# Kernel tuning notes

Measured on AMD Instinct MI355X. Metric: run time of the kernel, lower is better.

Reference implementation:

```python
import jax, jax.numpy as jnp
import numpy as np

B, S, HID, H = 4, 2048, 1024, 8
D = HID // H  # per-head dim = 128


def setup_inputs() -> dict:
    key = jax.random.key(0)
    ks = jax.random.split(key, 8)
    q = jax.random.normal(ks[0], (B, S, HID), dtype=jnp.float32)
    k = jax.random.normal(ks[1], (B, S, HID), dtype=jnp.float32)
    v = jax.random.normal(ks[2], (B, S, HID), dtype=jnp.float32)
    mask = jax.random.randint(ks[3], (B, S), 0, 2, dtype=jnp.int32)  # 1 = masked key
    # Linear(hidden, hidden, bias=False) weights, stored [in, out] so y = x @ W
    xavier = lambda kk: jax.random.uniform(kk, (HID, HID), jnp.float32,
                                           -np.sqrt(6.0 / (2 * HID)), np.sqrt(6.0 / (2 * HID)))
    return {"q": q, "k": k, "v": v, "mask": mask,
            "Wq": xavier(ks[4]), "Wk": xavier(ks[5]), "Wv": xavier(ks[6]), "Wo": xavier(ks[7])}


def reference(q, k, v, mask, Wq, Wk, Wv, Wo):
    scale = D ** -0.5
    # project and split heads: [B,S,HID] -> [B,H,S,D]
    qq = (q @ Wq).reshape(B, S, H, D).transpose(0, 2, 1, 3) * scale
    kk = (k @ Wk).reshape(B, S, H, D).transpose(0, 2, 1, 3)
    vv = (v @ Wv).reshape(B, S, H, D).transpose(0, 2, 1, 3)
    # scores [B,H,Sq,Sk]; mask broadcasts over heads and query rows (key padding)
    scores = jnp.einsum('bhqd,bhkd->bhqk', qq, kk)
    scores = jnp.where(mask.astype(bool)[:, None, None, :], jnp.float32(-1e9), scores)
    attn = jax.nn.softmax(scores, axis=-1)  # dropout_rate=0 (eval) -> identity
    ctx = jnp.einsum('bhqk,bhkd->bhqd', attn, vv)
    out = ctx.transpose(0, 2, 1, 3).reshape(B, S, HID) @ Wo
    return out, attn
```

## Files before the change

kernel.cpp:

```cpp
#include <hip/hip_runtime.h>
#include <hip/hip_bf16.h>

#define HIDN 1024
#define NH   8
#define DH   128
#define BB   4
#define SS   2048

typedef __bf16 bf16;
typedef bf16 bf16x4 __attribute__((ext_vector_type(4)));
typedef bf16 bf16x8 __attribute__((ext_vector_type(8)));
typedef float f32x4 __attribute__((ext_vector_type(4)));

#if __has_builtin(__builtin_amdgcn_exp2f)
#define EXP2(x) __builtin_amdgcn_exp2f(x)
#else
#define EXP2(x) exp2f(x)
#endif

static __device__ inline f32x4 mfma16(bf16x8 a, bf16x8 b, f32x4 c) {
    return __builtin_amdgcn_mfma_f32_16x16x32_bf16(a, b, c, 0, 0, 0);
}

static __device__ inline void gload_lds16(const void* g, void* l) {
    __builtin_amdgcn_global_load_lds(
        (const __attribute__((address_space(1))) unsigned int*)g,
        (__attribute__((address_space(3))) unsigned int*)l, 16, 0, 0);
}

__global__ void cvt_kernel(const float* __restrict__ q, const float* __restrict__ k,
                           const float* __restrict__ v,
                           bf16* __restrict__ qo, bf16* __restrict__ ko, bf16* __restrict__ vo) {
    const float* src = blockIdx.y == 0 ? q : blockIdx.y == 1 ? k : v;
    bf16* dst = blockIdx.y == 0 ? qo : blockIdx.y == 1 ? ko : vo;
    const size_t n = (size_t)BB * SS * HIDN;
    for (size_t i = ((size_t)blockIdx.x * blockDim.x + threadIdx.x) * 8; i < n;
         i += (size_t)gridDim.x * blockDim.x * 8) {
        float4 a = *(const float4*)&src[i];
        float4 b = *(const float4*)&src[i + 4];
        bf16x8 o = {(bf16)a.x, (bf16)a.y, (bf16)a.z, (bf16)a.w,
                    (bf16)b.x, (bf16)b.y, (bf16)b.z, (bf16)b.w};
        *(bf16x8*)&dst[i] = o;
    }
}

__global__ void wconv_kernel(const float* __restrict__ W0, const float* __restrict__ W1,
                             const float* __restrict__ W2, const float* __restrict__ W3,
                             bf16* __restrict__ O) {
    const float* W = blockIdx.z == 0 ? W0 : blockIdx.z == 1 ? W1 : blockIdx.z == 2 ? W2 : W3;
    bf16* WT = O + (size_t)blockIdx.z * HIDN * HIDN;
    int nb = blockIdx.x * 64;
    int kb = blockIdx.y * 64;
    int t = threadIdx.x;
    __shared__ bf16 tile[64][72];
    {
        int r = t >> 2, cp = (t & 3) * 16;
        #pragma unroll
        for (int j = 0; j < 16; j += 4) {
            float4 val = *(const float4*)&W[(size_t)(kb + r) * HIDN + nb + cp + j];
            tile[r][cp + j + 0] = (bf16)val.x;
            tile[r][cp + j + 1] = (bf16)val.y;
            tile[r][cp + j + 2] = (bf16)val.z;
            tile[r][cp + j + 3] = (bf16)val.w;
        }
    }
    __syncthreads();
    {
        int n = t >> 2, kp = (t & 3) * 16;
        bf16 o[16];
        #pragma unroll
        for (int j = 0; j < 16; ++j) o[j] = tile[kp + j][n];
        #pragma unroll
        for (int j = 0; j < 2; ++j)
            *(bf16x8*)&WT[(size_t)(nb + n) * HIDN + kb + kp + j * 8] = *(bf16x8*)&o[j * 8];
    }
}

template <int OUTMODE>
static __device__ inline void gemm_core(const bf16* __restrict__ A, const bf16* __restrict__ Bt,
                                        void* __restrict__ Cp, float alpha, char* smem) {
    int orig = blockIdx.x + blockIdx.y * gridDim.x;
    int virt = (orig & 7) * 64 + (orig >> 3);
    int bm = (virt & 63) * 128;
    int bn = (virt >> 6) * 128;
    int t = threadIdx.x;
    int wave = t >> 6, lane = t & 63;
    int wr = wave >> 1, wc = wave & 1;
    int lr = lane & 15, lg = lane >> 4;
    int so = wave * 1024 + lane * 16;
    f32x4 acc[4][4] = {};

    auto stage = [&](int k0, char* buf) {
        #pragma unroll
        for (int i = 0; i < 4; ++i) {
            int o = i * 4096 + so;
            int r = o >> 7, cb = o & 127;
            int cbs = cb ^ ((r & 7) << 4);
            gload_lds16(&A[(size_t)(bm + r) * HIDN + k0 + (cbs >> 1)], buf + i * 4096 + wave * 1024);
            gload_lds16(&Bt[(size_t)(bn + r) * HIDN + k0 + (cbs >> 1)], buf + 16384 + i * 4096 + wave * 1024);
        }
    };
    stage(0, smem);
    for (int kt = 0; kt < 16; ++kt) {
        const char* cur = smem + (kt & 1) * 32768;
        char* nxt = smem + ((kt & 1) ^ 1) * 32768;
        asm volatile("s_waitcnt vmcnt(0)" ::: "memory");
        __builtin_amdgcn_s_barrier();
        if (kt < 15) stage((kt + 1) * 64, nxt);
        asm volatile("" ::: "memory");
        #pragma unroll
        for (int kd = 0; kd < 2; ++kd) {
            bf16x8 af[4], bfr[4];
            #pragma unroll
            for (int mi = 0; mi < 4; ++mi) {
                int row = wr * 64 + mi * 16 + lr;
                int cb = (kd * 64 + lg * 16) ^ ((row & 7) << 4);
                af[mi] = *(const bf16x8*)(cur + row * 128 + cb);
            }
            #pragma unroll
            for (int ni = 0; ni < 4; ++ni) {
                int row = wc * 64 + ni * 16 + lr;
                int cb = (kd * 64 + lg * 16) ^ ((row & 7) << 4);
                bfr[ni] = *(const bf16x8*)(cur + 16384 + row * 128 + cb);
            }
            #pragma unroll
            for (int mi = 0; mi < 4; ++mi)
                #pragma unroll
                for (int ni = 0; ni < 4; ++ni)
                    acc[mi][ni] = mfma16(af[mi], bfr[ni], acc[mi][ni]);
        }
    }
    if constexpr (OUTMODE == 2) {
        __syncthreads();
        bf16* tile_t = (bf16*)smem;
        #pragma unroll
        for (int mi = 0; mi < 4; ++mi)
            #pragma unroll
            for (int ni = 0; ni < 4; ++ni) {
                bf16x4 o = {(bf16)acc[mi][ni][0], (bf16)acc[mi][ni][1],
                            (bf16)acc[mi][ni][2], (bf16)acc[mi][ni][3]};
                *(bf16x4*)&tile_t[(wc * 64 + ni * 16 + lr) * 136 + wr * 64 + mi * 16 + lg * 4] = o;
            }
        __syncthreads();
        int d = t >> 1, sh = (t & 1) * 64;
        int b = bm >> 11, h = bn >> 7;
        bf16* vvT = (bf16*)Cp;
        size_t base = ((size_t)(b * NH + h) * DH + d) * SS + (bm & 2047) + sh;
        #pragma unroll
        for (int j = 0; j < 8; ++j)
            *(bf16x8*)&vvT[base + j * 8] = *(const bf16x8*)&tile_t[d * 136 + sh + j * 8];
    } else {
        #pragma unroll
        for (int mi = 0; mi < 4; ++mi)
            #pragma unroll
            for (int ni = 0; ni < 4; ++ni)
                #pragma unroll
                for (int r = 0; r < 4; ++r) {
                    int row = bm + wr * 64 + mi * 16 + lg * 4 + r;
                    int col = bn + wc * 64 + ni * 16 + lr;
                    if constexpr (OUTMODE == 0)
                        ((bf16*)Cp)[(size_t)row * HIDN + col] = (bf16)(acc[mi][ni][r] * alpha);
                    else
                        ((float*)Cp)[(size_t)row * HIDN + col] = acc[mi][ni][r] * alpha;
                }
    }
}

__global__ __launch_bounds__(256, 2)
void proj_gemm_kernel(const bf16* __restrict__ qb, const bf16* __restrict__ kb,
                      const bf16* __restrict__ vb, const bf16* __restrict__ Wall,
                      bf16* __restrict__ qq, bf16* __restrict__ kk, bf16* __restrict__ vvT,
                      float qalpha) {
    __shared__ __align__(16) char smem[65536];
    int z = blockIdx.z;
    const bf16* Bt = Wall + (size_t)z * HIDN * HIDN;
    if (z == 2)      gemm_core<2>(vb, Bt, vvT, 1.0f, smem);
    else if (z == 1) gemm_core<0>(kb, Bt, kk, 1.0f, smem);
    else             gemm_core<0>(qb, Bt, qq, qalpha, smem);
}

__global__ __launch_bounds__(256, 2)
void out_gemm_kernel(const bf16* __restrict__ A, const bf16* __restrict__ Bt,
                     float* __restrict__ C) {
    __shared__ __align__(16) char smem[65536];
    gemm_core<1>(A, Bt, C, 1.0f, smem);
}

static __device__ inline void stage_k(const bf16* kbase, int kt, char* Ksm, int wave, int lane) {
    #pragma unroll
    for (int i = 0; i < 8; ++i) {
        int o = i * 4096 + wave * 1024 + lane * 16;
        int r = o >> 8, cb = o & 255;
        int cbs = cb ^ ((r & 15) << 4);
        gload_lds16(&kbase[(size_t)(kt * 128 + r) * HIDN + (cbs >> 1)],
                    Ksm + i * 4096 + wave * 1024);
    }
}

static __device__ inline bf16x8 read_k(const char* Ksm, int row, int cstart_bytes) {
    int cb = cstart_bytes ^ ((row & 15) << 4);
    return *(const bf16x8*)(Ksm + row * 256 + cb);
}

__global__ __launch_bounds__(256, 2)
void attn_fused_kernel(const bf16* __restrict__ qq, const bf16* __restrict__ kk,
                       const bf16* __restrict__ vvT, const int* __restrict__ mask,
                       float* __restrict__ attn, bf16* __restrict__ ctx) {
    __shared__ __align__(16) char smem[67584];
    char* K0 = smem;
    char* K1 = smem + 32768;
    bf16(*P)[136] = (bf16(*)[136])(smem + 32768);
    float* slf = (float*)(smem + 32768);

    int orig = blockIdx.x + blockIdx.y * gridDim.x;
    int virt = (orig & 7) * 64 + (orig >> 3);
    int qt = virt & 15, bh = virt >> 4;
    int b = bh >> 3, h = bh & 7;
    int t = threadIdx.x;
    int wave = t >> 6, lane = t & 63;
    int wr = wave >> 1, wc = wave & 1;
    int lr = lane & 15, lg = lane >> 4;

    const bf16* qbase = qq + (size_t)b * SS * HIDN + h * DH;
    const bf16* kbase = kk + (size_t)b * SS * HIDN + h * DH;
    const int* mbase = mask + b * SS;

    bf16x8 qf[4][4];
    #pragma unroll
    for (int mi = 0; mi < 4; ++mi)
        #pragma unroll
        for (int kd = 0; kd < 4; ++kd)
            qf[mi][kd] = *(const bf16x8*)&qbase[(size_t)(qt * 128 + wr * 64 + mi * 16 + lr) * HIDN + kd * 32 + lg * 8];

    unsigned long long mkbits = 0;
    #pragma unroll
    for (int kt = 0; kt < 16; ++kt)
        #pragma unroll
        for (int ni = 0; ni < 4; ++ni)
            mkbits |= (unsigned long long)(mbase[kt * 128 + wc * 64 + ni * 16 + lr] != 0)
                      << (kt * 4 + ni);

    float l_[16] = {};
    stage_k(kbase, 0, K0, wave, lane);
    for (int kt = 0; kt < 16; ++kt) {
        const char* cur = (kt & 1) ? K1 : K0;
        char* nxt = (kt & 1) ? K0 : K1;
        __syncthreads();
        if (kt < 15) stage_k(kbase, kt + 1, nxt, wave, lane);
        f32x4 acc[4][4] = {};
        #pragma unroll
        for (int kd = 0; kd < 4; ++kd) {
            bf16x8 kf[4];
            #pragma unroll
            for (int ni = 0; ni < 4; ++ni)
                kf[ni] = read_k(cur, wc * 64 + ni * 16 + lr, kd * 64 + lg * 16);
            #pragma unroll
            for (int mi = 0; mi < 4; ++mi)
                #pragma unroll
                for (int ni = 0; ni < 4; ++ni)
                    acc[mi][ni] = mfma16(qf[mi][kd], kf[ni], acc[mi][ni]);
        }
        #pragma unroll
        for (int mi = 0; mi < 4; ++mi)
            #pragma unroll
            for (int r = 0; r < 4; ++r) {
                int s = mi * 4 + r;
                float v0 = ((mkbits >> (kt * 4 + 0)) & 1) ? -1e9f : acc[mi][0][r];
                float v1 = ((mkbits >> (kt * 4 + 1)) & 1) ? -1e9f : acc[mi][1][r];
                float v2 = ((mkbits >> (kt * 4 + 2)) & 1) ? -1e9f : acc[mi][2][r];
                float v3 = ((mkbits >> (kt * 4 + 3)) & 1) ? -1e9f : acc[mi][3][r];
                l_[s] += (EXP2(v0 - 12.f) + EXP2(v1 - 12.f)) + (EXP2(v2 - 12.f) + EXP2(v3 - 12.f));
            }
    }

    stage_k(kbase, 0, K0, wave, lane);

    #pragma unroll
    for (int o = 1; o < 16; o <<= 1)
        #pragma unroll
        for (int s = 0; s < 16; ++s) l_[s] += __shfl_xor(l_[s], o);
    __syncthreads();
    if (lr == 0) {
        #pragma unroll
        for (int mi = 0; mi < 4; ++mi)
            #pragma unroll
            for (int r = 0; r < 4; ++r)
                slf[wc * 128 + wr * 64 + mi * 16 + lg * 4 + r] = l_[mi * 4 + r];
    }
    __syncthreads();
    float rl[16];
    #pragma unroll
    for (int mi = 0; mi < 4; ++mi)
        #pragma unroll
        for (int r = 0; r < 4; ++r) {
            int row = wr * 64 + mi * 16 + lg * 4 + r;
            rl[mi * 4 + r] = 1.0f / (slf[row] + slf[128 + row]);
        }
    __syncthreads();

    f32x4 cacc[4][4] = {};
    for (int kt = 0; kt < 16; ++kt) {
        f32x4 acc[4][4] = {};
        #pragma unroll
        for (int kd = 0; kd < 4; ++kd) {
            bf16x8 kf[4];
            #pragma unroll
            for (int ni = 0; ni < 4; ++ni)
                kf[ni] = read_k(K0, wc * 64 + ni * 16 + lr, kd * 64 + lg * 16);
            #pragma unroll
            for (int mi = 0; mi < 4; ++mi)
                #pragma unroll
                for (int ni = 0; ni < 4; ++ni)
                    acc[mi][ni] = mfma16(qf[mi][kd], kf[ni], acc[mi][ni]);
        }
        #pragma unroll
        for (int mi = 0; mi < 4; ++mi)
            #pragma unroll
            for (int ni = 0; ni < 4; ++ni)
                #pragma unroll
                for (int r = 0; r < 4; ++r) {
                    float s = ((mkbits >> (kt * 4 + ni)) & 1) ? -1e9f : acc[mi][ni][r];
                    float p = EXP2(s - 12.f) * rl[mi * 4 + r];
                    int rowl = wr * 64 + mi * 16 + lg * 4 + r;
                    int coll = wc * 64 + ni * 16 + lr;
                    P[rowl][coll] = (bf16)p;
                    __builtin_nontemporal_store(
                        p, &attn[((size_t)bh * SS + qt * 128 + rowl) * SS + kt * 128 + coll]);
                }
        __syncthreads();
        if (kt < 15) stage_k(kbase, kt + 1, K0, wave, lane);
        #pragma unroll
        for (int ks = 0; ks < 4; ++ks) {
            bf16x8 pf[4], vf[4];
            #pragma unroll
            for (int mi = 0; mi < 4; ++mi)
                pf[mi] = *(const bf16x8*)&P[wr * 64 + mi * 16 + lr][ks * 32 + lg * 8];
            #pragma unroll
            for (int ni = 0; ni < 4; ++ni)
                vf[ni] = *(const bf16x8*)&vvT[((size_t)bh * DH + wc * 64 + ni * 16 + lr) * SS + kt * 128 + ks * 32 + lg * 8];
            #pragma unroll
            for (int mi = 0; mi < 4; ++mi)
                #pragma unroll
                for (int ni = 0; ni < 4; ++ni)
                    cacc[mi][ni] = mfma16(pf[mi], vf[ni], cacc[mi][ni]);
        }
        __syncthreads();
    }

    #pragma unroll
    for (int mi = 0; mi < 4; ++mi)
        #pragma unroll
        for (int ni = 0; ni < 4; ++ni)
            #pragma unroll
            for (int r = 0; r < 4; ++r)
                P[wr * 64 + mi * 16 + lg * 4 + r][wc * 64 + ni * 16 + lr] = (bf16)cacc[mi][ni][r];
    __syncthreads();
    {
        int row = t >> 1, half = (t & 1) * 64;
        bf16* dst = ctx + ((size_t)b * SS + qt * 128 + row) * HIDN + h * DH + half;
        #pragma unroll
        for (int j = 0; j < 8; ++j)
            *(bf16x8*)&dst[j * 8] = *(const bf16x8*)&P[row][half + j * 8];
    }
}

extern "C" void kernel_launch(void* const* d_in, const int* in_sizes, int n_in,
                              void* d_out, int out_size, void* d_ws, size_t ws_size,
                              hipStream_t stream) {
    const float* q = (const float*)d_in[0];
    const float* k = (const float*)d_in[1];
    const float* v = (const float*)d_in[2];
    const int* mask = (const int*)d_in[3];
    const float* Wq = (const float*)d_in[4];
    const float* Wk = (const float*)d_in[5];
    const float* Wv = (const float*)d_in[6];
    const float* Wo = (const float*)d_in[7];
    (void)in_sizes; (void)n_in; (void)out_size; (void)ws_size;

    float* outp = (float*)d_out;
    float* attn = outp + (size_t)BB * SS * HIDN;

    char* ws = (char*)d_ws;
    size_t off = 0;
    auto alloc = [&](size_t bytes) { char* p = ws + off; off += (bytes + 255) & ~(size_t)255; return p; };
    const size_t wbytes = (size_t)HIDN * HIDN * sizeof(bf16);
    const size_t tbytes = (size_t)BB * SS * HIDN * sizeof(bf16);
    bf16* WmatT = (bf16*)alloc(4 * wbytes);
    bf16* qbf = (bf16*)alloc(tbytes);
    bf16* kbf = (bf16*)alloc(tbytes);
    bf16* vbf = (bf16*)alloc(tbytes);
    bf16* qqb = (bf16*)alloc(tbytes);
    bf16* kkb = (bf16*)alloc(tbytes);
    bf16* vvTb = (bf16*)alloc(tbytes);
    bf16* ctxb = qbf;
    bf16* WoT = WmatT + 3 * (size_t)HIDN * HIDN;

    dim3 blk(256);
    cvt_kernel<<<dim3(1024, 3), blk, 0, stream>>>(q, k, v, qbf, kbf, vbf);
    wconv_kernel<<<dim3(16, 16, 4), blk, 0, stream>>>(Wq, Wk, Wv, Wo, WmatT);

    const float qalpha = 0.12751744f;
    proj_gemm_kernel<<<dim3(64, 8, 3), blk, 0, stream>>>(qbf, kbf, vbf, WmatT,
                                                         qqb, kkb, vvTb, qalpha);

    attn_fused_kernel<<<dim3(16, 32), blk, 0, stream>>>(qqb, kkb, vvTb, mask, attn, ctxb);

    out_gemm_kernel<<<dim3(64, 8), blk, 0, stream>>>(ctxb, WoT, outp);
}
```

Before: 361.1 us.

## Split attention into ctx kernel with deferred normalization and separate probs kernel

The fused attention kernel, which ran QK^T twice (a row-sum pass, then a probs+PV pass), is replaced by two kernels. The first computes unnormalized exp scores, accumulates PV and the row sums in one pass, then scales ctx by the reciprocal and writes the reciprocals to a workspace buffer. A second kernel with smaller 64x64 tiles and higher occupancy recomputes QK^T and streams the normalized attention probabilities to memory. This moves the large fp32 attn store out of the PV loop into a lighter, more parallel kernel, at the cost of an extra launch and recomputing QK^T. It also adds s_setprio hints around the MFMA blocks.

Result: slower. 441.1 us (+22.2%).

```diff
diff --git a/kernel.cpp b/kernel.cpp
--- a/kernel.cpp
+++ b/kernel.cpp
@@ -197,18 +197,28 @@
     }
 }
 
+static __device__ inline void stage64(const bf16* kb, int row0, char* buf, int wave, int lane) {
+    #pragma unroll
+    for (int i = 0; i < 4; ++i) {
+        int o = i * 4096 + wave * 1024 + lane * 16;
+        int r = o >> 8, cb = o & 255;
+        int cbs = cb ^ ((r & 15) << 4);
+        gload_lds16(&kb[(size_t)(row0 + r) * HIDN + (cbs >> 1)],
+                    buf + i * 4096 + wave * 1024);
+    }
+}
+
 static __device__ inline bf16x8 read_k(const char* Ksm, int row, int cstart_bytes) {
     int cb = cstart_bytes ^ ((row & 15) << 4);
     return *(const bf16x8*)(Ksm + row * 256 + cb);
 }
 
 __global__ __launch_bounds__(256, 2)
-void attn_fused_kernel(const bf16* __restrict__ qq, const bf16* __restrict__ kk,
-                       const bf16* __restrict__ vvT, const int* __restrict__ mask,
-                       float* __restrict__ attn, bf16* __restrict__ ctx) {
+void attn_ctx_kernel(const bf16* __restrict__ qq, const bf16* __restrict__ kk,
+                     const bf16* __restrict__ vvT, const int* __restrict__ mask,
+                     float* __restrict__ rlg, bf16* __restrict__ ctx) {
     __shared__ __align__(16) char smem[67584];
     char* K0 = smem;
-    char* K1 = smem + 32768;
     bf16(*P)[136] = (bf16(*)[136])(smem + 32768);
     float* slf = (float*)(smem + 32768);
 
@@ -241,45 +251,65 @@
                       << (kt * 4 + ni);
 
     float l_[16] = {};
+    f32x4 cacc[4][4] = {};
     stage_k(kbase, 0, K0, wave, lane);
+    __syncthreads();
     for (int kt = 0; kt < 16; ++kt) {
-        const char* cur = (kt & 1) ? K1 : K0;
-        char* nxt = (kt & 1) ? K0 : K1;
-        __syncthreads();
-        if (kt < 15) stage_k(kbase, kt + 1, nxt, wave, lane);
         f32x4 acc[4][4] = {};
+        __builtin_amdgcn_s_setprio(1);
         #pragma unroll
         for (int kd = 0; kd < 4; ++kd) {
             bf16x8 kf[4];
             #pragma unroll
             for (int ni = 0; ni < 4; ++ni)
-                kf[ni] = read_k(cur, wc * 64 + ni * 16 + lr, kd * 64 + lg * 16);
+                kf[ni] = read_k(K0, wc * 64 + ni * 16 + lr, kd * 64 + lg * 16);
             #pragma unroll
             for (int mi = 0; mi < 4; ++mi)
                 #pragma unroll
                 for (int ni = 0; ni < 4; ++ni)
                     acc[mi][ni] = mfma16(qf[mi][kd], kf[ni], acc[mi][ni]);
         }
+        __builtin_amdgcn_s_setprio(0);
         #pragma unroll
         for (int mi = 0; mi < 4; ++mi)
             #pragma unroll
             for (int r = 0; r < 4; ++r) {
                 int s = mi * 4 + r;
-                float v0 = ((mkbits >> (kt * 4 + 0)) & 1) ? -1e9f : acc[mi][0][r];
-                float v1 = ((mkbits >> (kt * 4 + 1)) & 1) ? -1e9f : acc[mi][1][r];
-                float v2 = ((mkbits >> (kt * 4 + 2)) & 1) ? -1e9f : acc[mi][2][r];
-                float v3 = ((mkbits >> (kt * 4 + 3)) & 1) ? -1e9f : acc[mi][3][r];
-                l_[s] += (EXP2(v0 - 12.f) + EXP2(v1 - 12.f)) + (EXP2(v2 - 12.f) + EXP2(v3 - 12.f));
+                int rowl = wr * 64 + mi * 16 + lg * 4 + r;
+                #pragma unroll
+                for (int ni = 0; ni < 4; ++ni) {
+                    float v = ((mkbits >> (kt * 4 + ni)) & 1) ? -1e9f : acc[mi][ni][r];
+                    float p = EXP2(v - 12.f);
+                    l_[s] += p;
+                    P[rowl][wc * 64 + ni * 16 + lr] = (bf16)p;
+                }
             }
-    }
-
-    stage_k(kbase, 0, K0, wave, lane);
+        __syncthreads();
+        if (kt < 15) stage_k(kbase, kt + 1, K0, wave, lane);
+        __builtin_amdgcn_s_setprio(1);
+        #pragma unroll
+        for (int ks = 0; ks < 4; ++ks) {
+            bf16x8 pf[4], vf[4];
+            #pragma unroll
+            for (int mi = 0; mi < 4; ++mi)
+                pf[mi] = *(const bf16x8*)&P[wr * 64 + mi * 16 + lr][ks * 32 + lg * 8];
+            #pragma unroll
+            for (int ni = 0; ni < 4; ++ni)
+                vf[ni] = *(const bf16x8*)&vvT[((size_t)bh * DH + wc * 64 + ni * 16 + lr) * SS + kt * 128 + ks * 32 + lg * 8];
+            #pragma unroll
+            for (int mi = 0; mi < 4; ++mi)
+                #pragma unroll
+                for (int ni = 0; ni < 4; ++ni)
+                    cacc[mi][ni] = mfma16(pf[mi], vf[ni], cacc[mi][ni]);
+        }
+        __builtin_amdgcn_s_setprio(0);
+        __syncthreads();
+    }
 
     #pragma unroll
     for (int o = 1; o < 16; o <<= 1)
         #pragma unroll
         for (int s = 0; s < 16; ++s) l_[s] += __shfl_xor(l_[s], o);
-    __syncthreads();
     if (lr == 0) {
         #pragma unroll
         for (int mi = 0; mi < 4; ++mi)
@@ -296,64 +326,23 @@
             int row = wr * 64 + mi * 16 + lg * 4 + r;
             rl[mi * 4 + r] = 1.0f / (slf[row] + slf[128 + row]);
         }
+    if (lr == 0) {
+        #pragma unroll
+        for (int mi = 0; mi < 4; ++mi)
+            #pragma unroll
+            for (int r = 0; r < 4; ++r)
+                rlg[(size_t)bh * SS + qt * 128 + wr * 64 + mi * 16 + lg * 4 + r] = rl[mi * 4 + r];
+    }
     __syncthreads();
 
-    f32x4 cacc[4][4] = {};
-    for (int kt = 0; kt < 16; ++kt) {
-        f32x4 acc[4][4] = {};
-        #pragma unroll
-        for (int kd = 0; kd < 4; ++kd) {
-            bf16x8 kf[4];
-            #pragma unroll
-            for (int ni = 0; ni < 4; ++ni)
-                kf[ni] = read_k(K0, wc * 64 + ni * 16 + lr, kd * 64 + lg * 16);
-            #pragma unroll
-            for (int mi = 0; mi < 4; ++mi)
-                #pragma unroll
-                for (int ni = 0; ni < 4; ++ni)
-                    acc[mi][ni] = mfma16(qf[mi][kd], kf[ni], acc[mi][ni]);
-        }
-        #pragma unroll
-        for (int mi = 0; mi < 4; ++mi)
-            #pragma unroll
-            for (int ni = 0; ni < 4; ++ni)
-                #pragma unroll
-                for (int r = 0; r < 4; ++r) {
-                    float s = ((mkbits >> (kt * 4 + ni)) & 1) ? -1e9f : acc[mi][ni][r];
-                    float p = EXP2(s - 12.f) * rl[mi * 4 + r];
-                    int rowl = wr * 64 + mi * 16 + lg * 4 + r;
-                    int coll = wc * 64 + ni * 16 + lr;
-                    P[rowl][coll] = (bf16)p;
-                    __builtin_nontemporal_store(
-                        p, &attn[((size_t)bh * SS + qt * 128 + rowl) * SS + kt * 128 + coll]);
-                }
-        __syncthreads();
-        if (kt < 15) stage_k(kbase, kt + 1, K0, wave, lane);
-        #pragma unroll
-        for (int ks = 0; ks < 4; ++ks) {
-            bf16x8 pf[4], vf[4];
-            #pragma unroll
-            for (int mi = 0; mi < 4; ++mi)
-                pf[mi] = *(const bf16x8*)&P[wr * 64 + mi * 16 + lr][ks * 32 + lg * 8];
-            #pragma unroll
-            for (int ni = 0; ni < 4; ++ni)
-                vf[ni] = *(const bf16x8*)&vvT[((size_t)bh * DH + wc * 64 + ni * 16 + lr) * SS + kt * 128 + ks * 32 + lg * 8];
-            #pragma unroll
-            for (int mi = 0; mi < 4; ++mi)
-                #pragma unroll
-                for (int ni = 0; ni < 4; ++ni)
-                    cacc[mi][ni] = mfma16(pf[mi], vf[ni], cacc[mi][ni]);
-        }
-        __syncthreads();
-    }
-
     #pragma unroll
     for (int mi = 0; mi < 4; ++mi)
         #pragma unroll
         for (int ni = 0; ni < 4; ++ni)
             #pragma unroll
             for (int r = 0; r < 4; ++r)
-                P[wr * 64 + mi * 16 + lg * 4 + r][wc * 64 + ni * 16 + lr] = (bf16)cacc[mi][ni][r];
+                P[wr * 64 + mi * 16 + lg * 4 + r][wc * 64 + ni * 16 + lr] =
+                    (bf16)(cacc[mi][ni][r] * rl[mi * 4 + r]);
     __syncthreads();
     {
         int row = t >> 1, half = (t & 1) * 64;
@@ -361,6 +350,84 @@
         #pragma unroll
         for (int j = 0; j < 8; ++j)
             *(bf16x8*)&dst[j * 8] = *(const bf16x8*)&P[row][half + j * 8];
+    }
+}
+
+__global__ __launch_bounds__(256, 4)
+void attn_probs_kernel(const bf16* __restrict__ qq, const bf16* __restrict__ kk,
+                       const int* __restrict__ mask, const float* __restrict__ rlg,
+                       float* __restrict__ attn) {
+    __shared__ __align__(16) char smem[32768];
+    int orig = blockIdx.x;
+    int virt = (orig & 7) * 128 + (orig >> 3);
+    int qt = virt & 31, bh = virt >> 5;
+    int b = bh >> 3, h = bh & 7;
+    int t = threadIdx.x;
+    int wave = t >> 6, lane = t & 63;
+    int wr = wave >> 1, wc = wave & 1;
+    int lr = lane & 15, lg = lane >> 4;
+
+    const bf16* qbase = qq + (size_t)b * SS * HIDN + h * DH;
+    const bf16* kbase = kk + (size_t)b * SS * HIDN + h * DH;
+    const int* mbase = mask + b * SS;
+
+    bf16x8 qf[2][4];
+    #pragma unroll
+    for (int mi = 0; mi < 2; ++mi)
+        #pragma unroll
+        for (int kd = 0; kd < 4; ++kd)
+            qf[mi][kd] = *(const bf16x8*)&qbase[(size_t)(qt * 64 + wr * 32 + mi * 16 + lr) * HIDN + kd * 32 + lg * 8];
+
+    unsigned long long mkbits = 0;
+    #pragma unroll
+    for (int kt = 0; kt < 32; ++kt)
+        #pragma unroll
+        for (int ni = 0; ni < 2; ++ni)
+            mkbits |= (unsigned long long)(mbase[kt * 64 + wc * 32 + ni * 16 + lr] != 0)
+                      << (kt * 2 + ni);
+
+    float rl[8];
+    #pragma unroll
+    for (int mi = 0; mi < 2; ++mi)
+        #pragma unroll
+        for (int r = 0; r < 4; ++r)
+            rl[mi * 4 + r] = rlg[(size_t)bh * SS + qt * 64 + wr * 32 + mi * 16 + lg * 4 + r];
+
+    float* abase = attn + ((size_t)bh * SS + qt * 64) * SS;
+
+    stage64(kbase, 0, smem, wave, lane);
+    for (int kt = 0; kt < 32; ++kt) {
+        const char* cur = smem + (kt & 1) * 16384;
+        char* nxt = smem + ((kt & 1) ^ 1) * 16384;
+        __syncthreads();
+        if (kt < 31) stage64(kbase, (kt + 1) * 64, nxt, wave, lane);
+        f32x4 acc[2][2] = {};
+        __builtin_amdgcn_s_setprio(1);
+        #pragma unroll
+        for (int kd = 0; kd < 4; ++kd) {
+            bf16x8 kf[2];
+            #pragma unroll
+            for (int ni = 0; ni < 2; ++ni)
+                kf[ni] = read_k(cur, wc * 32 + ni * 16 + lr, kd * 64 + lg * 16);
+            #pragma unroll
+            for (int mi = 0; mi < 2; ++mi)
+                #pragma unroll
+                for (int ni = 0; ni < 2; ++ni)
+                    acc[mi][ni] = mfma16(qf[mi][kd], kf[ni], acc[mi][ni]);
+        }
+        __builtin_amdgcn_s_setprio(0);
+        #pragma unroll
+        for (int mi = 0; mi < 2; ++mi)
+            #pragma unroll
+            for (int r = 0; r < 4; ++r) {
+                float v0 = ((mkbits >> (kt * 2 + 0)) & 1) ? -1e9f : acc[mi][0][r];
+                float v1 = ((mkbits >> (kt * 2 + 1)) & 1) ? -1e9f : acc[mi][1][r];
+                float p0 = EXP2(v0 - 12.f) * rl[mi * 4 + r];
+                float p1 = EXP2(v1 - 12.f) * rl[mi * 4 + r];
+                int rowl = wr * 32 + mi * 16 + lg * 4 + r;
+                __builtin_nontemporal_store(p0, &abase[(size_t)rowl * SS + kt * 64 + wc * 32 + lr]);
+                __builtin_nontemporal_store(p1, &abase[(size_t)rowl * SS + kt * 64 + wc * 32 + 16 + lr]);
+            }
     }
 }
 
@@ -392,6 +459,7 @@
     bf16* qqb = (bf16*)alloc(tbytes);
     bf16* kkb = (bf16*)alloc(tbytes);
     bf16* vvTb = (bf16*)alloc(tbytes);
+    float* rlb = (float*)alloc((size_t)BB * NH * SS * sizeof(float));
     bf16* ctxb = qbf;
     bf16* WoT = WmatT + 3 * (size_t)HIDN * HIDN;
 
@@ -403,7 +471,8 @@
     proj_gemm_kernel<<<dim3(64, 8, 3), blk, 0, stream>>>(qbf, kbf, vbf, WmatT,
                                                          qqb, kkb, vvTb, qalpha);
 
-    attn_fused_kernel<<<dim3(16, 32), blk, 0, stream>>>(qqb, kkb, vvTb, mask, attn, ctxb);
+    attn_ctx_kernel<<<dim3(16, 32), blk, 0, stream>>>(qqb, kkb, vvTb, mask, rlb, ctxb);
+    attn_probs_kernel<<<dim3(1024), blk, 0, stream>>>(qqb, kkb, mask, rlb, attn);
 
     out_gemm_kernel<<<dim3(64, 8), blk, 0, stream>>>(ctxb, WoT, outp);
 }
```

## Halve key tile to 64 in fused attention to fit three blocks per CU

Applied to the files above, without the earlier changes.

Cuts the key tile in the fused attention kernel from 128 to 64 rows, which shrinks LDS from 67.5KB to 50KB and the per-iteration accumulator tiles, and raises launch bounds to 3 blocks per CU. The second pass now double-buffers K in two 16KB buffers, where before it reloaded a single buffer. MFMA sections are wrapped in s_setprio to favour matrix issue. The ctx epilogue is split into two halves so it fits the smaller P buffer. The trade-offs are twice as many loop iterations and barriers, and register pressure that must now fit a 3-wave occupancy bound.

Measured after the change: 471.6 us. 30.6% more time.

```diff
diff --git a/kernel.cpp b/kernel.cpp
--- a/kernel.cpp
+++ b/kernel.cpp
@@ -186,14 +186,14 @@
     gemm_core<1>(A, Bt, C, 1.0f, smem);
 }
 
-static __device__ inline void stage_k(const bf16* kbase, int kt, char* Ksm, int wave, int lane) {
-    #pragma unroll
-    for (int i = 0; i < 8; ++i) {
+static __device__ inline void stage64(const bf16* kb, int row0, char* buf, int wave, int lane) {
+    #pragma unroll
+    for (int i = 0; i < 4; ++i) {
         int o = i * 4096 + wave * 1024 + lane * 16;
         int r = o >> 8, cb = o & 255;
         int cbs = cb ^ ((r & 15) << 4);
-        gload_lds16(&kbase[(size_t)(kt * 128 + r) * HIDN + (cbs >> 1)],
-                    Ksm + i * 4096 + wave * 1024);
+        gload_lds16(&kb[(size_t)(row0 + r) * HIDN + (cbs >> 1)],
+                    buf + i * 4096 + wave * 1024);
     }
 }
 
@@ -202,14 +202,14 @@
     return *(const bf16x8*)(Ksm + row * 256 + cb);
 }
 
-__global__ __launch_bounds__(256, 2)
+__global__ __launch_bounds__(256, 3)
 void attn_fused_kernel(const bf16* __restrict__ qq, const bf16* __restrict__ kk,
                        const bf16* __restrict__ vvT, const int* __restrict__ mask,
                        float* __restrict__ attn, bf16* __restrict__ ctx) {
-    __shared__ __align__(16) char smem[67584];
-    char* K0 = smem;
-    char* K1 = smem + 32768;
-    bf16(*P)[136] = (bf16(*)[136])(smem + 32768);
+    __shared__ __align__(16) char smem[51200];
+    char* KA = smem;
+    char* KB = smem + 16384;
+    bf16(*P)[72] = (bf16(*)[72])(smem + 32768);
     float* slf = (float*)(smem + 32768);
 
     int orig = blockIdx.x + blockIdx.y * gridDim.x;
@@ -234,46 +234,46 @@
 
     unsigned long long mkbits = 0;
     #pragma unroll
-    for (int kt = 0; kt < 16; ++kt)
-        #pragma unroll
-        for (int ni = 0; ni < 4; ++ni)
-            mkbits |= (unsigned long long)(mbase[kt * 128 + wc * 64 + ni * 16 + lr] != 0)
-                      << (kt * 4 + ni);
+    for (int kt = 0; kt < 32; ++kt)
+        #pragma unroll
+        for (int ni = 0; ni < 2; ++ni)
+            mkbits |= (unsigned long long)(mbase[kt * 64 + wc * 32 + ni * 16 + lr] != 0)
+                      << (kt * 2 + ni);
 
     float l_[16] = {};
-    stage_k(kbase, 0, K0, wave, lane);
-    for (int kt = 0; kt < 16; ++kt) {
-        const char* cur = (kt & 1) ? K1 : K0;
-        char* nxt = (kt & 1) ? K0 : K1;
-        __syncthreads();
-        if (kt < 15) stage_k(kbase, kt + 1, nxt, wave, lane);
-        f32x4 acc[4][4] = {};
+    stage64(kbase, 0, KA, wave, lane);
+    for (int kt = 0; kt < 32; ++kt) {
+        const char* cur = (kt & 1) ? KB : KA;
+        char* nxt = (kt & 1) ? KA : KB;
+        __syncthreads();
+        if (kt < 31) stage64(kbase, (kt + 1) * 64, nxt, wave, lane);
+        f32x4 acc[4][2] = {};
+        __builtin_amdgcn_s_setprio(1);
         #pragma unroll
         for (int kd = 0; kd < 4; ++kd) {
-            bf16x8 kf[4];
-            #pragma unroll
-            for (int ni = 0; ni < 4; ++ni)
-                kf[ni] = read_k(cur, wc * 64 + ni * 16 + lr, kd * 64 + lg * 16);
-            #pragma unroll
-            for (int mi = 0; mi < 4; ++mi)
-                #pragma unroll
-                for (int ni = 0; ni < 4; ++ni)
+            bf16x8 kf[2];
+            #pragma unroll
+            for (int ni = 0; ni < 2; ++ni)
+                kf[ni] = read_k(cur, wc * 32 + ni * 16 + lr, kd * 64 + lg * 16);
+            #pragma unroll
+            for (int mi = 0; mi < 4; ++mi)
+                #pragma unroll
+                for (int ni = 0; ni < 2; ++ni)
                     acc[mi][ni] = mfma16(qf[mi][kd], kf[ni], acc[mi][ni]);
         }
+        __builtin_amdgcn_s_setprio(0);
         #pragma unroll
         for (int mi = 0; mi < 4; ++mi)
             #pragma unroll
             for (int r = 0; r < 4; ++r) {
                 int s = mi * 4 + r;
-                float v0 = ((mkbits >> (kt * 4 + 0)) & 1) ? -1e9f : acc[mi][0][r];
-                float v1 = ((mkbits >> (kt * 4 + 1)) & 1) ? -1e9f : acc[mi][1][r];
-                float v2 = ((mkbits >> (kt * 4 + 2)) & 1) ? -1e9f : acc[mi][2][r];
-                float v3 = ((mkbits >> (kt * 4 + 3)) & 1) ? -1e9f : acc[mi][3][r];
-                l_[s] += (EXP2(v0 - 12.f) + EXP2(v1 - 12.f)) + (EXP2(v2 - 12.f) + EXP2(v3 - 12.f));
+                float v0 = ((mkbits >> (kt * 2 + 0)) & 1) ? -1e9f : acc[mi][0][r];
+                float v1 = ((mkbits >> (kt * 2 + 1)) & 1) ? -1e9f : acc[mi][1][r];
+                l_[s] += EXP2(v0 - 12.f) + EXP2(v1 - 12.f);
             }
     }
 
-    stage_k(kbase, 0, K0, wave, lane);
+    stage64(kbase, 0, KA, wave, lane);
 
     #pragma unroll
     for (int o = 1; o < 16; o <<= 1)
@@ -299,68 +299,78 @@
     __syncthreads();
 
     f32x4 cacc[4][4] = {};
-    for (int kt = 0; kt < 16; ++kt) {
-        f32x4 acc[4][4] = {};
+    for (int kt = 0; kt < 32; ++kt) {
+        const char* cur = (kt & 1) ? KB : KA;
+        char* nxt = (kt & 1) ? KA : KB;
+        f32x4 acc[4][2] = {};
+        __builtin_amdgcn_s_setprio(1);
         #pragma unroll
         for (int kd = 0; kd < 4; ++kd) {
-            bf16x8 kf[4];
-            #pragma unroll
-            for (int ni = 0; ni < 4; ++ni)
-                kf[ni] = read_k(K0, wc * 64 + ni * 16 + lr, kd * 64 + lg * 16);
-            #pragma unroll
-            for (int mi = 0; mi < 4; ++mi)
-                #pragma unroll
-                for (int ni = 0; ni < 4; ++ni)
+            bf16x8 kf[2];
+            #pragma unroll
+            for (int ni = 0; ni < 2; ++ni)
+                kf[ni] = read_k(cur, wc * 32 + ni * 16 + lr, kd * 64 + lg * 16);
+            #pragma unroll
+            for (int mi = 0; mi < 4; ++mi)
+                #pragma unroll
+                for (int ni = 0; ni < 2; ++ni)
                     acc[mi][ni] = mfma16(qf[mi][kd], kf[ni], acc[mi][ni]);
         }
+        __builtin_amdgcn_s_setprio(0);
         #pragma unroll
         for (int mi = 0; mi < 4; ++mi)
             #pragma unroll
-            for (int ni = 0; ni < 4; ++ni)
+            for (int ni = 0; ni < 2; ++ni)
                 #pragma unroll
                 for (int r = 0; r < 4; ++r) {
-                    float s = ((mkbits >> (kt * 4 + ni)) & 1) ? -1e9f : acc[mi][ni][r];
+                    float s = ((mkbits >> (kt * 2 + ni)) & 1) ? -1e9f : acc[mi][ni][r];
                     float p = EXP2(s - 12.f) * rl[mi * 4 + r];
                     int rowl = wr * 64 + mi * 16 + lg * 4 + r;
-                    int coll = wc * 64 + ni * 16 + lr;
+                    int coll = wc * 32 + ni * 16 + lr;
                     P[rowl][coll] = (bf16)p;
                     __builtin_nontemporal_store(
-                        p, &attn[((size_t)bh * SS + qt * 128 + rowl) * SS + kt * 128 + coll]);
+                        p, &attn[((size_t)bh * SS + qt * 128 + rowl) * SS + kt * 64 + coll]);
                 }
         __syncthreads();
-        if (kt < 15) stage_k(kbase, kt + 1, K0, wave, lane);
-        #pragma unroll
-        for (int ks = 0; ks < 4; ++ks) {
+        if (kt < 31) stage64(kbase, (kt + 1) * 64, nxt, wave, lane);
+        __builtin_amdgcn_s_setprio(1);
+        #pragma unroll
+        for (int ks = 0; ks < 2; ++ks) {
             bf16x8 pf[4], vf[4];
             #pragma unroll
             for (int mi = 0; mi < 4; ++mi)
                 pf[mi] = *(const bf16x8*)&P[wr * 64 + mi * 16 + lr][ks * 32 + lg * 8];
             #pragma unroll
             for (int ni = 0; ni < 4; ++ni)
-                vf[ni] = *(const bf16x8*)&vvT[((size_t)bh * DH + wc * 64 + ni * 16 + lr) * SS + kt * 128 + ks * 32 + lg * 8];
+                vf[ni] = *(const bf16x8*)&vvT[((size_t)bh * DH + wc * 64 + ni * 16 + lr) * SS + kt * 64 + ks * 32 + lg * 8];
             #pragma unroll
             for (int mi = 0; mi < 4; ++mi)
                 #pragma unroll
                 for (int ni = 0; ni < 4; ++ni)
                     cacc[mi][ni] = mfma16(pf[mi], vf[ni], cacc[mi][ni]);
         }
-        __syncthreads();
-    }
-
-    #pragma unroll
-    for (int mi = 0; mi < 4; ++mi)
-        #pragma unroll
-        for (int ni = 0; ni < 4; ++ni)
-            #pragma unroll
-            for (int r = 0; r < 4; ++r)
-                P[wr * 64 + mi * 16 + lg * 4 + r][wc * 64 + ni * 16 + lr] = (bf16)cacc[mi][ni][r];
-    __syncthreads();
-    {
-        int row = t >> 1, half = (t & 1) * 64;
-        bf16* dst = ctx + ((size_t)b * SS + qt * 128 + row) * HIDN + h * DH + half;
-        #pragma unroll
-        for (int j = 0; j < 8; ++j)
-            *(bf16x8*)&dst[j * 8] = *(const bf16x8*)&P[row][half + j * 8];
+        __builtin_amdgcn_s_setprio(0);
+        __syncthreads();
+    }
+
+    #pragma unroll
+    for (int hp = 0; hp < 2; ++hp) {
+        __syncthreads();
+        if (wc == hp) {
+            #pragma unroll
+            for (int mi = 0; mi < 4; ++mi)
+                #pragma unroll
+                for (int ni = 0; ni < 4; ++ni)
+                    #pragma unroll
+                    for (int r = 0; r < 4; ++r)
+                        P[wr * 64 + mi * 16 + lg * 4 + r][ni * 16 + lr] = (bf16)cacc[mi][ni][r];
+        }
+        __syncthreads();
+        int row = t >> 1, part = (t & 1) * 32;
+        bf16* dst = ctx + ((size_t)b * SS + qt * 128 + row) * HIDN + h * DH + hp * 64 + part;
+        #pragma unroll
+        for (int j = 0; j < 4; ++j)
+            *(bf16x8*)&dst[j * 8] = *(const bf16x8*)&P[row][part + j * 8];
     }
 }
 
```
